# Kernel optimization log

Hardware: AMD Instinct MI355X
Metric: run time of the kernel (lower is better)

Reference implementation:

```python
import jax, jax.numpy as jnp
import numpy as np

K = 0.001  # sigmoid temperature from DGCLoss init
EPS = 1e-8


def _off_diag(m):
    # [..., n, n] -> [..., n, n-1], removing the diagonal in row-major order
    n = m.shape[-1]
    lead = m.shape[:-2]
    flat = m.reshape(lead + (n * n,))[..., :-1]
    return flat.reshape(lead + (n - 1, n + 1))[..., 1:].reshape(lead + (n, n - 1))


def setup_inputs() -> dict:
    key = jax.random.key(0)
    k1, k2 = jax.random.split(key)
    ranking = jax.random.normal(k1, (384, 256), dtype=jnp.float32)
    gt = jax.random.randint(k2, (384,), 0, 6, dtype=jnp.int64)
    return {"ranking": ranking, "gt": gt}


def reference(ranking, gt):
    x = ranking
    N = x.shape[0]
    # cosine similarity matrix, mapped to [0, 1]
    xn = x / jnp.clip(jnp.linalg.norm(x, axis=1, keepdims=True), EPS, None)
    sm = (xn @ xn.T + 1.0) * 0.5                         # [N, N]
    rank = _off_diag(sm)                                 # [N, N-1]
    g = jnp.abs(gt[None, :] - gt[:, None]).astype(jnp.float32)  # [N, N]
    g = _off_diag(g)                                     # [N, N-1]
    M = N - 1
    # dij[n, i, j] = rank[n, j] - rank[n, i]
    dij = rank[:, None, :] - rank[:, :, None]            # [N, M, M]
    dij = _off_diag(dij)                                 # [N, M, M-1]
    # clamped sigmoid indicator
    indicator = 1.0 / (1.0 + jnp.exp(jnp.clip(-dij / K, -50.0, 50.0)))
    indicator = indicator.sum(-1) + 1.0                  # [N, M]
    relevance = jnp.exp2(jnp.clip(10.0 - g, 0.0, None)) - 1.0  # [N, M]
    dcg = (relevance / jnp.log2(indicator + 1.0)).sum(axis=1)  # [N]
    # ideal DCG from sorted relevance
    rel_sorted = jnp.sort(relevance, axis=-1)[:, ::-1]
    discount = jnp.log2(jnp.arange(M, dtype=jnp.float32) + 2.0)
    idcg = (rel_sorted / discount).sum(axis=-1)          # [N]
    valid = idcg != 0.0
    ndcg = jnp.where(valid, dcg / jnp.where(valid, idcg, 1.0), 0.0)
    cnt = valid.sum()
    mean_ndcg = ndcg.sum() / jnp.maximum(cnt, 1).astype(jnp.float32)
    return jnp.where(cnt == 0, jnp.float32(1.0), 1.0 - mean_ndcg)
```

## Files before the change

### kernel.cpp

```cpp
#include <hip/hip_runtime.h>


#define NN 384
#define DD 256
#define MM 383
#define HSCALE 721.3475204444817f
#define NBUCK  256
#define BSCALE 0.1767955801104972f
#define WWIN   6.0f

__global__ __launch_bounds__(256) void dgc_normT(const float* __restrict__ x,
                                                 const int* __restrict__ gt,
                                                 float* __restrict__ XT,
                                                 float* __restrict__ XN,
                                                 float* __restrict__ idcg_tab) {
    const int t = threadIdx.x;

    if (blockIdx.x == 24) {
        __shared__ int   cnt[6];
        __shared__ int   cum[6][6];
        __shared__ float wred[4][6];
        const int lane = t & 63;
        const int wave = t >> 6;

        if (t < 6) cnt[t] = 0;
        __syncthreads();
        atomicAdd(&cnt[gt[t]], 1);
        if (t + 256 < NN) atomicAdd(&cnt[gt[t + 256]], 1);
        __syncthreads();
        if (t < 6) {
            int h[6];
            #pragma unroll
            for (int g = 0; g < 6; ++g) h[g] = 0;
            #pragma unroll
            for (int v = 0; v < 6; ++v) {
                int d = v - t; d = d < 0 ? -d : d;
                h[d] += cnt[v];
            }
            h[0] -= 1;
            int s = 0;
            #pragma unroll
            for (int g = 0; g < 6; ++g) { s += h[g]; cum[t][g] = s; }
        }
        __syncthreads();

        float acc[6] = {0.f, 0.f, 0.f, 0.f, 0.f, 0.f};
        for (int p = t; p < MM; p += 256) {
            const float invl = 1.0f / __builtin_amdgcn_logf((float)(p + 2));
            #pragma unroll
            for (int gv = 0; gv < 6; ++gv) {
                const int g = (p >= cum[gv][0]) + (p >= cum[gv][1])
                            + (p >= cum[gv][2]) + (p >= cum[gv][3])
                            + (p >= cum[gv][4]);
                acc[gv] += (float)((1 << (10 - g)) - 1) * invl;
            }
        }
        for (int off = 32; off > 0; off >>= 1) {
            #pragma unroll
            for (int gv = 0; gv < 6; ++gv) acc[gv] += __shfl_down(acc[gv], off, 64);
        }
        if (lane == 0) {
            #pragma unroll
            for (int gv = 0; gv < 6; ++gv) wred[wave][gv] = acc[gv];
        }
        __syncthreads();
        if (t < 6) idcg_tab[t] = wred[0][t] + wred[1][t] + wred[2][t] + wred[3][t];
        return;
    }

    __shared__ float xs[16][260];
    __shared__ float invn[16];
    const int r0 = blockIdx.x * 16;

    #pragma unroll
    for (int i = 0; i < 4; ++i) {
        int f = t + i * 256;
        int r = f >> 6, c4 = f & 63;
        float4 v = ((const float4*)(x + (size_t)(r0 + r) * DD))[c4];
        xs[r][c4 * 4 + 0] = v.x; xs[r][c4 * 4 + 1] = v.y;
        xs[r][c4 * 4 + 2] = v.z; xs[r][c4 * 4 + 3] = v.w;
    }
    __syncthreads();

    {
        const int r = t >> 4, sub = t & 15;
        float s = 0.0f;
        #pragma unroll
        for (int m = 0; m < 16; ++m) {
            float v = xs[r][sub * 16 + m];
            s = fmaf(v, v, s);
        }
        #pragma unroll
        for (int off = 8; off > 0; off >>= 1) s += __shfl_xor(s, off, 64);
        if (sub == 0) invn[r] = __builtin_amdgcn_rsqf(fmaxf(s, 1e-16f));
    }
    __syncthreads();

    {
        const int r  = t & 15;
        const int kk = t >> 4;
        const float inv = invn[r];
        #pragma unroll
        for (int i = 0; i < 16; ++i) {
            int k = i * 16 + kk;
            XT[(size_t)k * NN + r0 + r] = xs[r][k] * inv;
        }
    }
    {
        #pragma unroll
        for (int i = 0; i < 4; ++i) {
            int f = t + i * 256;
            int r = f >> 6, c4 = f & 63;
            const float inv = invn[r];
            float4 v;
            v.x = xs[r][c4 * 4 + 0] * inv; v.y = xs[r][c4 * 4 + 1] * inv;
            v.z = xs[r][c4 * 4 + 2] * inv; v.w = xs[r][c4 * 4 + 3] * inv;
            ((float4*)(XN + (size_t)(r0 + r) * DD))[c4] = v;
        }
    }
}

__global__ __launch_bounds__(768) void dgc_fused(const float* __restrict__ XT,
                                                 const float* __restrict__ XN,
                                                 const int* __restrict__ gt,
                                                 const float* __restrict__ idcg_tab,
                                                 float* __restrict__ ndcg) {
    __shared__ float  xs[2][DD];
    __shared__ float4 pacc[2][8][96];
    __shared__ float  srow[2][NN];
    __shared__ float  vsort[2][NN];
    __shared__ int    sidx[2][NN];
    __shared__ int    hist[2][NBUCK];
    __shared__ int    pre[2][NBUCK + 1];
    __shared__ float  redd[12];

    const int n0   = blockIdx.x * 2;
    const int t    = threadIdx.x;
    const int lane = t & 63;
    const int wave = t >> 6;

    if (t < 128)
        ((float4*)xs[t >> 6])[t & 63] =
            ((const float4*)(XN + (size_t)(n0 + (t >> 6)) * DD))[t & 63];
    if (t < 512) ((int*)hist)[t] = 0;
    __syncthreads();

    {
        const int j4 = t % 96;
        const int kc = t / 96;
        const float4* XT4 = (const float4*)XT;
        float4 a0 = {0.f, 0.f, 0.f, 0.f};
        float4 a1 = {0.f, 0.f, 0.f, 0.f};
        const int k0 = kc * 32;
        #pragma unroll 8
        for (int m = 0; m < 32; ++m) {
            const int k = k0 + m;
            float4 b = XT4[(size_t)k * 96 + j4];
            float s0 = xs[0][k];
            float s1 = xs[1][k];
            a0.x = fmaf(s0, b.x, a0.x); a0.y = fmaf(s0, b.y, a0.y);
            a0.z = fmaf(s0, b.z, a0.z); a0.w = fmaf(s0, b.w, a0.w);
            a1.x = fmaf(s1, b.x, a1.x); a1.y = fmaf(s1, b.y, a1.y);
            a1.z = fmaf(s1, b.z, a1.z); a1.w = fmaf(s1, b.w, a1.w);
        }
        pacc[0][kc][j4] = a0;
        pacc[1][kc][j4] = a1;
    }
    __syncthreads();

    const int r = t / 384;
    const int u = t - r * 384;

    {
        const float* pf = (const float*)pacc[r];
        float dot = 0.0f;
        #pragma unroll
        for (int c = 0; c < 8; ++c) dot += pf[c * 384 + u];
        srow[r][u] = fmaf(dot, HSCALE, HSCALE);
    }
    __syncthreads();

    const float vraw = srow[r][u];
    int b = (int)(vraw * BSCALE);
    b = b < 0 ? 0 : (b > NBUCK - 1 ? NBUCK - 1 : b);
    const int slot = atomicAdd(&hist[r][b], 1);
    __syncthreads();

    if (wave == 0 || wave == 6) {
        const int rr = wave / 6;
        const int s0 = hist[rr][lane * 4 + 0], s1 = hist[rr][lane * 4 + 1];
        const int s2 = hist[rr][lane * 4 + 2], s3 = hist[rr][lane * 4 + 3];
        const int sum = s0 + s1 + s2 + s3;
        int inc = sum;
        #pragma unroll
        for (int off = 1; off < 64; off <<= 1) {
            int uu = __shfl_up(inc, off, 64);
            if (lane >= off) inc += uu;
        }
        const int base = inc - sum;
        pre[rr][lane * 4 + 0] = base;
        pre[rr][lane * 4 + 1] = base + s0;
        pre[rr][lane * 4 + 2] = base + s0 + s1;
        pre[rr][lane * 4 + 3] = base + s0 + s1 + s2;
        if (lane == 63) pre[rr][NBUCK] = inc;
    }
    __syncthreads();

    {
        const int pos = pre[r][b] + slot;
        vsort[r][pos] = vraw;
        sidx[r][pos]  = u;
    }
    __syncthreads();

    const int   nrow  = n0 + r;
    const float ri    = vsort[r][u];
    const int   iorig = sidx[r][u];
    const float sn    = srow[r][nrow];

    int Blo = (int)((ri - WWIN) * BSCALE);
    int Bhi = (int)((ri + WWIN) * BSCALE);
    Blo = Blo < 0 ? 0 : (Blo > NBUCK - 1 ? NBUCK - 1 : Blo);
    Bhi = Bhi < 0 ? 0 : (Bhi > NBUCK - 1 ? NBUCK - 1 : Bhi);
    const int lo = pre[r][Blo];
    const int hi = pre[r][Bhi + 1];

    float acc = 0.0f;
    int q = lo;
    for (; q + 2 <= hi; q += 2) {
        float a = __builtin_amdgcn_exp2f(ri - vsort[r][q]);
        float bb = __builtin_amdgcn_exp2f(ri - vsort[r][q + 1]);
        float e = a + bb;
        float f = a * bb;
        acc = fmaf(2.0f + e, __builtin_amdgcn_rcpf(1.0f + e + f), acc);
    }
    if (q < hi)
        acc += __builtin_amdgcn_rcpf(1.0f + __builtin_amdgcn_exp2f(ri - vsort[r][q]));
    float sum_all = (float)(NN - hi) + acc;

    int bn = (int)(sn * BSCALE);
    bn = bn < 0 ? 0 : (bn > NBUCK - 1 ? NBUCK - 1 : bn);
    float cd = 0.0f;
    if (bn > Bhi)       cd = 1.0f;
    else if (bn >= Blo) cd = __builtin_amdgcn_rcpf(1.0f + __builtin_amdgcn_exp2f(ri - sn));
    const float ind = 0.5f + sum_all - cd;

    float dcg_i = 0.0f;
    if (iorig != nrow) {
        const int gd = gt[iorig] - gt[nrow];
        const int gg = gd < 0 ? -gd : gd;
        dcg_i = (float)((1 << (10 - gg)) - 1) / __builtin_amdgcn_logf(ind + 1.0f);
    }

    #pragma unroll
    for (int off = 32; off > 0; off >>= 1) dcg_i += __shfl_down(dcg_i, off, 64);
    if (lane == 0) redd[wave] = dcg_i;
    __syncthreads();
    if (t == 0)
        ndcg[n0] = (redd[0] + redd[1] + redd[2] + redd[3] + redd[4] + redd[5])
                   / idcg_tab[gt[n0]];
    if (t == 384)
        ndcg[n0 + 1] = (redd[6] + redd[7] + redd[8] + redd[9] + redd[10] + redd[11])
                       / idcg_tab[gt[n0 + 1]];
}

__global__ __launch_bounds__(384) void dgc_final(const float* __restrict__ ndcg,
                                                 float* __restrict__ out) {
    __shared__ float red[6];
    const int t    = threadIdx.x;
    const int lane = t & 63;
    const int wave = t >> 6;
    float nd = ndcg[t];
    #pragma unroll
    for (int off = 32; off > 0; off >>= 1) nd += __shfl_down(nd, off, 64);
    if (lane == 0) red[wave] = nd;
    __syncthreads();
    if (t == 0) {
        float s = 0.0f;
        for (int w = 0; w < 6; ++w) s += red[w];
        out[0] = 1.0f - s / (float)NN;
    }
}

extern "C" void kernel_launch(void* const* d_in, const int* in_sizes, int n_in,
                              void* d_out, int out_size, void* d_ws, size_t ws_size,
                              hipStream_t stream) {
    const float* ranking = (const float*)d_in[0];
    const int*   gt      = (const int*)d_in[1];
    float*       out     = (float*)d_out;

    float* XT   = (float*)d_ws;
    float* XN   = XT + (size_t)DD * NN;
    float* ndcg = XN + (size_t)NN * DD;
    float* tab  = ndcg + NN;

    dgc_normT<<<25, 256, 0, stream>>>(ranking, gt, XT, XN, tab);
    dgc_fused<<<NN / 2, 768, 0, stream>>>(XT, XN, gt, tab, ndcg);
    dgc_final<<<1, 384, 0, stream>>>(ndcg, out);
}
```

Baseline: 69.40 us.

## Fuse normalization and IDCG computation into the main kernel, dropping the prep launch

Removes the separate normalize/transpose kernel. Each block now reads raw rows straight from the input, computes row norms on the fly (half the threads also accumulate squared norms) and scales the dot products by both inverse norms. The IDCG table is recomputed per block by waves that are otherwise idle during the prefix scan. This saves a kernel launch and the intermediate XT/XN global buffers. In exchange every block redoes the full 384x256 norm computation, and each thread reads a whole row (strided, uncoalesced) instead of coalesced transposed loads.

Result: slower. 83.47 us (+20.3%).

```diff
diff --git a/kernel.cpp b/kernel.cpp
--- a/kernel.cpp
+++ b/kernel.cpp
@@ -9,178 +9,88 @@
 #define BSCALE 0.1767955801104972f
 #define WWIN   6.0f
 
-__global__ __launch_bounds__(256) void dgc_normT(const float* __restrict__ x,
+__global__ __launch_bounds__(768) void dgc_fused(const float* __restrict__ x,
                                                  const int* __restrict__ gt,
-                                                 float* __restrict__ XT,
-                                                 float* __restrict__ XN,
-                                                 float* __restrict__ idcg_tab) {
-    const int t = threadIdx.x;
-
-    if (blockIdx.x == 24) {
-        __shared__ int   cnt[6];
-        __shared__ int   cum[6][6];
-        __shared__ float wred[4][6];
-        const int lane = t & 63;
-        const int wave = t >> 6;
-
-        if (t < 6) cnt[t] = 0;
-        __syncthreads();
-        atomicAdd(&cnt[gt[t]], 1);
-        if (t + 256 < NN) atomicAdd(&cnt[gt[t + 256]], 1);
-        __syncthreads();
-        if (t < 6) {
-            int h[6];
-            #pragma unroll
-            for (int g = 0; g < 6; ++g) h[g] = 0;
-            #pragma unroll
-            for (int v = 0; v < 6; ++v) {
-                int d = v - t; d = d < 0 ? -d : d;
-                h[d] += cnt[v];
-            }
-            h[0] -= 1;
-            int s = 0;
-            #pragma unroll
-            for (int g = 0; g < 6; ++g) { s += h[g]; cum[t][g] = s; }
-        }
-        __syncthreads();
-
-        float acc[6] = {0.f, 0.f, 0.f, 0.f, 0.f, 0.f};
-        for (int p = t; p < MM; p += 256) {
-            const float invl = 1.0f / __builtin_amdgcn_logf((float)(p + 2));
-            #pragma unroll
-            for (int gv = 0; gv < 6; ++gv) {
-                const int g = (p >= cum[gv][0]) + (p >= cum[gv][1])
-                            + (p >= cum[gv][2]) + (p >= cum[gv][3])
-                            + (p >= cum[gv][4]);
-                acc[gv] += (float)((1 << (10 - g)) - 1) * invl;
-            }
-        }
-        for (int off = 32; off > 0; off >>= 1) {
-            #pragma unroll
-            for (int gv = 0; gv < 6; ++gv) acc[gv] += __shfl_down(acc[gv], off, 64);
-        }
-        if (lane == 0) {
-            #pragma unroll
-            for (int gv = 0; gv < 6; ++gv) wred[wave][gv] = acc[gv];
-        }
-        __syncthreads();
-        if (t < 6) idcg_tab[t] = wred[0][t] + wred[1][t] + wred[2][t] + wred[3][t];
-        return;
-    }
-
-    __shared__ float xs[16][260];
-    __shared__ float invn[16];
-    const int r0 = blockIdx.x * 16;
-
-    #pragma unroll
-    for (int i = 0; i < 4; ++i) {
-        int f = t + i * 256;
-        int r = f >> 6, c4 = f & 63;
-        float4 v = ((const float4*)(x + (size_t)(r0 + r) * DD))[c4];
-        xs[r][c4 * 4 + 0] = v.x; xs[r][c4 * 4 + 1] = v.y;
-        xs[r][c4 * 4 + 2] = v.z; xs[r][c4 * 4 + 3] = v.w;
-    }
-    __syncthreads();
-
-    {
-        const int r = t >> 4, sub = t & 15;
-        float s = 0.0f;
-        #pragma unroll
-        for (int m = 0; m < 16; ++m) {
-            float v = xs[r][sub * 16 + m];
-            s = fmaf(v, v, s);
-        }
-        #pragma unroll
-        for (int off = 8; off > 0; off >>= 1) s += __shfl_xor(s, off, 64);
-        if (sub == 0) invn[r] = __builtin_amdgcn_rsqf(fmaxf(s, 1e-16f));
-    }
-    __syncthreads();
-
-    {
-        const int r  = t & 15;
-        const int kk = t >> 4;
-        const float inv = invn[r];
-        #pragma unroll
-        for (int i = 0; i < 16; ++i) {
-            int k = i * 16 + kk;
-            XT[(size_t)k * NN + r0 + r] = xs[r][k] * inv;
-        }
-    }
-    {
-        #pragma unroll
-        for (int i = 0; i < 4; ++i) {
-            int f = t + i * 256;
-            int r = f >> 6, c4 = f & 63;
-            const float inv = invn[r];
-            float4 v;
-            v.x = xs[r][c4 * 4 + 0] * inv; v.y = xs[r][c4 * 4 + 1] * inv;
-            v.z = xs[r][c4 * 4 + 2] * inv; v.w = xs[r][c4 * 4 + 3] * inv;
-            ((float4*)(XN + (size_t)(r0 + r) * DD))[c4] = v;
-        }
-    }
-}
-
-__global__ __launch_bounds__(768) void dgc_fused(const float* __restrict__ XT,
-                                                 const float* __restrict__ XN,
-                                                 const int* __restrict__ gt,
-                                                 const float* __restrict__ idcg_tab,
                                                  float* __restrict__ ndcg) {
-    __shared__ float  xs[2][DD];
-    __shared__ float4 pacc[2][8][96];
-    __shared__ float  srow[2][NN];
-    __shared__ float  vsort[2][NN];
-    __shared__ int    sidx[2][NN];
-    __shared__ int    hist[2][NBUCK];
-    __shared__ int    pre[2][NBUCK + 1];
-    __shared__ float  redd[12];
+    __shared__ float xs[2][DD];
+    __shared__ float invn[NN];
+    __shared__ float srow[2][NN];
+    __shared__ float vsort[2][NN];
+    __shared__ int   sidx[2][NN];
+    __shared__ int   hist[2][NBUCK];
+    __shared__ int   pre[2][NBUCK + 1];
+    __shared__ int   cnt[6];
+    __shared__ int   cum[2][6];
+    __shared__ float redd[12];
+    __shared__ float idr[12][2];
 
     const int n0   = blockIdx.x * 2;
     const int t    = threadIdx.x;
     const int lane = t & 63;
     const int wave = t >> 6;
+    const int r    = t / 384;
+    const int u    = t - r * 384;
 
     if (t < 128)
         ((float4*)xs[t >> 6])[t & 63] =
-            ((const float4*)(XN + (size_t)(n0 + (t >> 6)) * DD))[t & 63];
+            ((const float4*)(x + (size_t)(n0 + (t >> 6)) * DD))[t & 63];
     if (t < 512) ((int*)hist)[t] = 0;
-    __syncthreads();
-
+    if (t < 6)  cnt[t] = 0;
+    if (t < 24) ((float*)idr)[t] = 0.0f;
+    __syncthreads();
+
+    if (t < NN) atomicAdd(&cnt[gt[t]], 1);
+
+    float dot;
     {
-        const int j4 = t % 96;
-        const int kc = t / 96;
-        const float4* XT4 = (const float4*)XT;
-        float4 a0 = {0.f, 0.f, 0.f, 0.f};
-        float4 a1 = {0.f, 0.f, 0.f, 0.f};
-        const int k0 = kc * 32;
-        #pragma unroll 8
-        for (int m = 0; m < 32; ++m) {
-            const int k = k0 + m;
-            float4 b = XT4[(size_t)k * 96 + j4];
-            float s0 = xs[0][k];
-            float s1 = xs[1][k];
-            a0.x = fmaf(s0, b.x, a0.x); a0.y = fmaf(s0, b.y, a0.y);
-            a0.z = fmaf(s0, b.z, a0.z); a0.w = fmaf(s0, b.w, a0.w);
-            a1.x = fmaf(s1, b.x, a1.x); a1.y = fmaf(s1, b.y, a1.y);
-            a1.z = fmaf(s1, b.z, a1.z); a1.w = fmaf(s1, b.w, a1.w);
-        }
-        pacc[0][kc][j4] = a0;
-        pacc[1][kc][j4] = a1;
-    }
-    __syncthreads();
-
-    const int r = t / 384;
-    const int u = t - r * 384;
-
-    {
-        const float* pf = (const float*)pacc[r];
-        float dot = 0.0f;
-        #pragma unroll
-        for (int c = 0; c < 8; ++c) dot += pf[c * 384 + u];
-        srow[r][u] = fmaf(dot, HSCALE, HSCALE);
-    }
-    __syncthreads();
-
-    const float vraw = srow[r][u];
+        const float4* xrow = (const float4*)(x + (size_t)u * DD);
+        const float4* xsr  = (const float4*)xs[r];
+        float4 ad = {0.f, 0.f, 0.f, 0.f};
+        if (r == 0) {
+            float4 as = {0.f, 0.f, 0.f, 0.f};
+            #pragma unroll 8
+            for (int k4 = 0; k4 < 64; ++k4) {
+                float4 bv = xrow[k4];
+                float4 av = xsr[k4];
+                ad.x = fmaf(av.x, bv.x, ad.x); ad.y = fmaf(av.y, bv.y, ad.y);
+                ad.z = fmaf(av.z, bv.z, ad.z); ad.w = fmaf(av.w, bv.w, ad.w);
+                as.x = fmaf(bv.x, bv.x, as.x); as.y = fmaf(bv.y, bv.y, as.y);
+                as.z = fmaf(bv.z, bv.z, as.z); as.w = fmaf(bv.w, bv.w, as.w);
+            }
+            const float sq = (as.x + as.y) + (as.z + as.w);
+            invn[u] = __builtin_amdgcn_rsqf(fmaxf(sq, 1e-16f));
+        } else {
+            #pragma unroll 8
+            for (int k4 = 0; k4 < 64; ++k4) {
+                float4 bv = xrow[k4];
+                float4 av = xsr[k4];
+                ad.x = fmaf(av.x, bv.x, ad.x); ad.y = fmaf(av.y, bv.y, ad.y);
+                ad.z = fmaf(av.z, bv.z, ad.z); ad.w = fmaf(av.w, bv.w, ad.w);
+            }
+        }
+        dot = (ad.x + ad.y) + (ad.z + ad.w);
+    }
+    __syncthreads();
+
+    if (t < 2) {
+        const int gv = gt[n0 + t];
+        int h[6];
+        #pragma unroll
+        for (int g = 0; g < 6; ++g) h[g] = 0;
+        #pragma unroll
+        for (int v = 0; v < 6; ++v) {
+            int d = v - gv; d = d < 0 ? -d : d;
+            h[d] += cnt[v];
+        }
+        h[0] -= 1;
+        int s = 0;
+        #pragma unroll
+        for (int g = 0; g < 6; ++g) { s += h[g]; cum[t][g] = s; }
+    }
+
+    const float cosn = dot * invn[u] * invn[n0 + r];
+    const float vraw = fmaf(cosn, HSCALE, HSCALE);
+    srow[r][u] = vraw;
     int b = (int)(vraw * BSCALE);
     b = b < 0 ? 0 : (b > NBUCK - 1 ? NBUCK - 1 : b);
     const int slot = atomicAdd(&hist[r][b], 1);
@@ -203,6 +113,25 @@
         pre[rr][lane * 4 + 2] = base + s0 + s1;
         pre[rr][lane * 4 + 3] = base + s0 + s1 + s2;
         if (lane == 63) pre[rr][NBUCK] = inc;
+    } else {
+        const int p = (wave < 6) ? (wave - 1) * 64 + lane
+                                 : 320 + (wave - 7) * 64 + lane;
+        float a0 = 0.0f, a1 = 0.0f;
+        if (p < MM) {
+            const float invl = 1.0f / __builtin_amdgcn_logf((float)(p + 2));
+            const int g0 = (p >= cum[0][0]) + (p >= cum[0][1]) + (p >= cum[0][2])
+                         + (p >= cum[0][3]) + (p >= cum[0][4]);
+            const int g1 = (p >= cum[1][0]) + (p >= cum[1][1]) + (p >= cum[1][2])
+                         + (p >= cum[1][3]) + (p >= cum[1][4]);
+            a0 = (float)((1 << (10 - g0)) - 1) * invl;
+            a1 = (float)((1 << (10 - g1)) - 1) * invl;
+        }
+        #pragma unroll
+        for (int off = 32; off > 0; off >>= 1) {
+            a0 += __shfl_down(a0, off, 64);
+            a1 += __shfl_down(a1, off, 64);
+        }
+        if (lane == 0) { idr[wave][0] = a0; idr[wave][1] = a1; }
     }
     __syncthreads();
 
@@ -228,7 +157,7 @@
     float acc = 0.0f;
     int q = lo;
     for (; q + 2 <= hi; q += 2) {
-        float a = __builtin_amdgcn_exp2f(ri - vsort[r][q]);
+        float a  = __builtin_amdgcn_exp2f(ri - vsort[r][q]);
         float bb = __builtin_amdgcn_exp2f(ri - vsort[r][q + 1]);
         float e = a + bb;
         float f = a * bb;
@@ -256,12 +185,17 @@
     for (int off = 32; off > 0; off >>= 1) dcg_i += __shfl_down(dcg_i, off, 64);
     if (lane == 0) redd[wave] = dcg_i;
     __syncthreads();
-    if (t == 0)
-        ndcg[n0] = (redd[0] + redd[1] + redd[2] + redd[3] + redd[4] + redd[5])
-                   / idcg_tab[gt[n0]];
-    if (t == 384)
-        ndcg[n0 + 1] = (redd[6] + redd[7] + redd[8] + redd[9] + redd[10] + redd[11])
-                       / idcg_tab[gt[n0 + 1]];
+
+    if (t == 0) {
+        const float id = idr[1][0] + idr[2][0] + idr[3][0] + idr[4][0] + idr[5][0]
+                       + idr[7][0] + idr[8][0] + idr[9][0] + idr[10][0] + idr[11][0];
+        ndcg[n0] = (redd[0] + redd[1] + redd[2] + redd[3] + redd[4] + redd[5]) / id;
+    }
+    if (t == 384) {
+        const float id = idr[1][1] + idr[2][1] + idr[3][1] + idr[4][1] + idr[5][1]
+                       + idr[7][1] + idr[8][1] + idr[9][1] + idr[10][1] + idr[11][1];
+        ndcg[n0 + 1] = (redd[6] + redd[7] + redd[8] + redd[9] + redd[10] + redd[11]) / id;
+    }
 }
 
 __global__ __launch_bounds__(384) void dgc_final(const float* __restrict__ ndcg,
@@ -289,12 +223,8 @@
     const int*   gt      = (const int*)d_in[1];
     float*       out     = (float*)d_out;
 
-    float* XT   = (float*)d_ws;
-    float* XN   = XT + (size_t)DD * NN;
-    float* ndcg = XN + (size_t)NN * DD;
-    float* tab  = ndcg + NN;
-
-    dgc_normT<<<25, 256, 0, stream>>>(ranking, gt, XT, XN, tab);
-    dgc_fused<<<NN / 2, 768, 0, stream>>>(XT, XN, gt, tab, ndcg);
+    float* ndcg = (float*)d_ws;
+
+    dgc_fused<<<NN / 2, 768, 0, stream>>>(ranking, gt, ndcg);
     dgc_final<<<1, 384, 0, stream>>>(ndcg, out);
 }
```

## Move IDCG computation into fused kernel and drop normalized row copy

Applied to the files above, without the earlier changes.

The first kernel no longer writes a normalized row-major copy of the input or computes the IDCG table in a separate block. It now emits only the transposed normalized matrix plus per-row inverse norms. The fused kernel rebuilds its two normalized rows from the raw input and the stored norm. It computes the IDCG for its two rows on the waves that sat idle during the prefix scan, using a per-block histogram of labels. This cuts global writes and the extra first-kernel block, but every block now repeats the 384-element label count and the IDCG work.

After: 69.81 us. Within noise of the previous version (+0.6%).

```diff
diff --git a/kernel.cpp b/kernel.cpp
--- a/kernel.cpp
+++ b/kernel.cpp
@@ -9,67 +9,12 @@
 #define BSCALE 0.1767955801104972f
 #define WWIN   6.0f
 
-__global__ __launch_bounds__(256) void dgc_normT(const float* __restrict__ x,
-                                                 const int* __restrict__ gt,
+__global__ __launch_bounds__(256) void dgc_trans(const float* __restrict__ x,
                                                  float* __restrict__ XT,
-                                                 float* __restrict__ XN,
-                                                 float* __restrict__ idcg_tab) {
-    const int t = threadIdx.x;
-
-    if (blockIdx.x == 24) {
-        __shared__ int   cnt[6];
-        __shared__ int   cum[6][6];
-        __shared__ float wred[4][6];
-        const int lane = t & 63;
-        const int wave = t >> 6;
-
-        if (t < 6) cnt[t] = 0;
-        __syncthreads();
-        atomicAdd(&cnt[gt[t]], 1);
-        if (t + 256 < NN) atomicAdd(&cnt[gt[t + 256]], 1);
-        __syncthreads();
-        if (t < 6) {
-            int h[6];
-            #pragma unroll
-            for (int g = 0; g < 6; ++g) h[g] = 0;
-            #pragma unroll
-            for (int v = 0; v < 6; ++v) {
-                int d = v - t; d = d < 0 ? -d : d;
-                h[d] += cnt[v];
-            }
-            h[0] -= 1;
-            int s = 0;
-            #pragma unroll
-            for (int g = 0; g < 6; ++g) { s += h[g]; cum[t][g] = s; }
-        }
-        __syncthreads();
-
-        float acc[6] = {0.f, 0.f, 0.f, 0.f, 0.f, 0.f};
-        for (int p = t; p < MM; p += 256) {
-            const float invl = 1.0f / __builtin_amdgcn_logf((float)(p + 2));
-            #pragma unroll
-            for (int gv = 0; gv < 6; ++gv) {
-                const int g = (p >= cum[gv][0]) + (p >= cum[gv][1])
-                            + (p >= cum[gv][2]) + (p >= cum[gv][3])
-                            + (p >= cum[gv][4]);
-                acc[gv] += (float)((1 << (10 - g)) - 1) * invl;
-            }
-        }
-        for (int off = 32; off > 0; off >>= 1) {
-            #pragma unroll
-            for (int gv = 0; gv < 6; ++gv) acc[gv] += __shfl_down(acc[gv], off, 64);
-        }
-        if (lane == 0) {
-            #pragma unroll
-            for (int gv = 0; gv < 6; ++gv) wred[wave][gv] = acc[gv];
-        }
-        __syncthreads();
-        if (t < 6) idcg_tab[t] = wred[0][t] + wred[1][t] + wred[2][t] + wred[3][t];
-        return;
-    }
-
+                                                 float* __restrict__ invn_g) {
     __shared__ float xs[16][260];
     __shared__ float invn[16];
+    const int t  = threadIdx.x;
     const int r0 = blockIdx.x * 16;
 
     #pragma unroll
@@ -96,6 +41,8 @@
     }
     __syncthreads();
 
+    if (t < 16) invn_g[r0 + t] = invn[t];
+
     {
         const int r  = t & 15;
         const int kk = t >> 4;
@@ -106,24 +53,12 @@
             XT[(size_t)k * NN + r0 + r] = xs[r][k] * inv;
         }
     }
-    {
-        #pragma unroll
-        for (int i = 0; i < 4; ++i) {
-            int f = t + i * 256;
-            int r = f >> 6, c4 = f & 63;
-            const float inv = invn[r];
-            float4 v;
-            v.x = xs[r][c4 * 4 + 0] * inv; v.y = xs[r][c4 * 4 + 1] * inv;
-            v.z = xs[r][c4 * 4 + 2] * inv; v.w = xs[r][c4 * 4 + 3] * inv;
-            ((float4*)(XN + (size_t)(r0 + r) * DD))[c4] = v;
-        }
-    }
 }
 
 __global__ __launch_bounds__(768) void dgc_fused(const float* __restrict__ XT,
-                                                 const float* __restrict__ XN,
+                                                 const float* __restrict__ x,
+                                                 const float* __restrict__ invn_g,
                                                  const int* __restrict__ gt,
-                                                 const float* __restrict__ idcg_tab,
                                                  float* __restrict__ ndcg) {
     __shared__ float  xs[2][DD];
     __shared__ float4 pacc[2][8][96];
@@ -132,18 +67,29 @@
     __shared__ int    sidx[2][NN];
     __shared__ int    hist[2][NBUCK];
     __shared__ int    pre[2][NBUCK + 1];
+    __shared__ int    cnt[6];
+    __shared__ int    cum[2][6];
     __shared__ float  redd[12];
+    __shared__ float  idr[12][2];
 
     const int n0   = blockIdx.x * 2;
     const int t    = threadIdx.x;
     const int lane = t & 63;
     const int wave = t >> 6;
 
-    if (t < 128)
-        ((float4*)xs[t >> 6])[t & 63] =
-            ((const float4*)(XN + (size_t)(n0 + (t >> 6)) * DD))[t & 63];
+    if (t < 128) {
+        const int rr = t >> 6;
+        const float inv = invn_g[n0 + rr];
+        float4 v = ((const float4*)(x + (size_t)(n0 + rr) * DD))[t & 63];
+        v.x *= inv; v.y *= inv; v.z *= inv; v.w *= inv;
+        ((float4*)xs[rr])[t & 63] = v;
+    }
     if (t < 512) ((int*)hist)[t] = 0;
-    __syncthreads();
+    if (t < 6)  cnt[t] = 0;
+    if (t < 24) ((float*)idr)[t] = 0.0f;
+    __syncthreads();
+
+    if (t < NN) atomicAdd(&cnt[gt[t]], 1);
 
     {
         const int j4 = t % 96;
@@ -171,6 +117,22 @@
     const int r = t / 384;
     const int u = t - r * 384;
 
+    if (t < 2) {
+        const int gv = gt[n0 + t];
+        int h[6];
+        #pragma unroll
+        for (int g = 0; g < 6; ++g) h[g] = 0;
+        #pragma unroll
+        for (int v = 0; v < 6; ++v) {
+            int d = v - gv; d = d < 0 ? -d : d;
+            h[d] += cnt[v];
+        }
+        h[0] -= 1;
+        int s = 0;
+        #pragma unroll
+        for (int g = 0; g < 6; ++g) { s += h[g]; cum[t][g] = s; }
+    }
+
     {
         const float* pf = (const float*)pacc[r];
         float dot = 0.0f;
@@ -203,6 +165,25 @@
         pre[rr][lane * 4 + 2] = base + s0 + s1;
         pre[rr][lane * 4 + 3] = base + s0 + s1 + s2;
         if (lane == 63) pre[rr][NBUCK] = inc;
+    } else {
+        const int p = (wave < 6) ? (wave - 1) * 64 + lane
+                                 : 320 + (wave - 7) * 64 + lane;
+        float a0 = 0.0f, a1 = 0.0f;
+        if (p < MM) {
+            const float invl = 1.0f / __builtin_amdgcn_logf((float)(p + 2));
+            const int g0 = (p >= cum[0][0]) + (p >= cum[0][1]) + (p >= cum[0][2])
+                         + (p >= cum[0][3]) + (p >= cum[0][4]);
+            const int g1 = (p >= cum[1][0]) + (p >= cum[1][1]) + (p >= cum[1][2])
+                         + (p >= cum[1][3]) + (p >= cum[1][4]);
+            a0 = (float)((1 << (10 - g0)) - 1) * invl;
+            a1 = (float)((1 << (10 - g1)) - 1) * invl;
+        }
+        #pragma unroll
+        for (int off = 32; off > 0; off >>= 1) {
+            a0 += __shfl_down(a0, off, 64);
+            a1 += __shfl_down(a1, off, 64);
+        }
+        if (lane == 0) { idr[wave][0] = a0; idr[wave][1] = a1; }
     }
     __syncthreads();
 
@@ -228,7 +209,7 @@
     float acc = 0.0f;
     int q = lo;
     for (; q + 2 <= hi; q += 2) {
-        float a = __builtin_amdgcn_exp2f(ri - vsort[r][q]);
+        float a  = __builtin_amdgcn_exp2f(ri - vsort[r][q]);
         float bb = __builtin_amdgcn_exp2f(ri - vsort[r][q + 1]);
         float e = a + bb;
         float f = a * bb;
@@ -256,12 +237,18 @@
     for (int off = 32; off > 0; off >>= 1) dcg_i += __shfl_down(dcg_i, off, 64);
     if (lane == 0) redd[wave] = dcg_i;
     __syncthreads();
-    if (t == 0)
-        ndcg[n0] = (redd[0] + redd[1] + redd[2] + redd[3] + redd[4] + redd[5])
-                   / idcg_tab[gt[n0]];
-    if (t == 384)
+
+    if (t == 0) {
+        const float id = idr[1][0] + idr[2][0] + idr[3][0] + idr[4][0] + idr[5][0]
+                       + idr[7][0] + idr[8][0] + idr[9][0] + idr[10][0] + idr[11][0];
+        ndcg[n0] = (redd[0] + redd[1] + redd[2] + redd[3] + redd[4] + redd[5]) / id;
+    }
+    if (t == 384) {
+        const float id = idr[1][1] + idr[2][1] + idr[3][1] + idr[4][1] + idr[5][1]
+                       + idr[7][1] + idr[8][1] + idr[9][1] + idr[10][1] + idr[11][1];
         ndcg[n0 + 1] = (redd[6] + redd[7] + redd[8] + redd[9] + redd[10] + redd[11])
-                       / idcg_tab[gt[n0 + 1]];
+                       / id;
+    }
 }
 
 __global__ __launch_bounds__(384) void dgc_final(const float* __restrict__ ndcg,
@@ -289,12 +276,11 @@
     const int*   gt      = (const int*)d_in[1];
     float*       out     = (float*)d_out;
 
-    float* XT   = (float*)d_ws;
-    float* XN   = XT + (size_t)DD * NN;
-    float* ndcg = XN + (size_t)NN * DD;
-    float* tab  = ndcg + NN;
-
-    dgc_normT<<<25, 256, 0, stream>>>(ranking, gt, XT, XN, tab);
-    dgc_fused<<<NN / 2, 768, 0, stream>>>(XT, XN, gt, tab, ndcg);
+    float* XT     = (float*)d_ws;
+    float* invn_g = XT + (size_t)DD * NN;
+    float* ndcg   = invn_g + NN;
+
+    dgc_trans<<<24, 256, 0, stream>>>(ranking, XT, invn_g);
+    dgc_fused<<<NN / 2, 768, 0, stream>>>(XT, ranking, invn_g, gt, ndcg);
     dgc_final<<<1, 384, 0, stream>>>(ndcg, out);
 }
```
